# Kernel optimization log

Hardware: AMD Instinct MI355X
Metric: run time of the kernel (lower is better)

## Reference

```python
import jax, jax.numpy as jnp
import numpy as np

G = 128          # dense grid extent per axis
N = 131072       # number of occupied voxels
MUL = 32         # multiplicity of 0e and 1o irreps
DIM = 4 * MUL    # 32 scalars + 32 vectors*3 = 128
NB = 5           # num_radial_basis
R = 2.5          # diameter / 2
K = 125          # 5^3 kernel offsets


def _lattice_constants():
    # 5x5x5 lattice of physical offsets (steps = 1.0)
    v = jnp.arange(-2.0, 3.0)
    xx, yy, zz = jnp.meshgrid(v, v, v, indexing='ij')
    lattice = jnp.stack([xx, yy, zz], -1)              # (5,5,5,3)
    norm = jnp.linalg.norm(lattice, axis=-1)           # (5,5,5)
    # soft_one_hot_linspace, basis='smooth_finite', cutoff=True
    values = jnp.linspace(0.0, R, NB + 2)[1:-1]
    step = R / (NB + 1)
    d = (norm[..., None] - values) / step              # (5,5,5,NB)
    inside = jnp.abs(d) < 1.0
    ds = jnp.clip(d, -1.0 + 1e-6, 1.0 - 1e-6)
    emb = jnp.where(inside, 1.14136 * jnp.exp(2.0 - 1.0 / (1.0 + ds) - 1.0 / (1.0 - ds)), 0.0)
    # spherical harmonics l=0,1, normalize=True, 'component' norm (e3nn l=1 order: y,z,x)
    unit = jnp.where(norm[..., None] > 0, lattice / jnp.maximum(norm, 1e-9)[..., None], 0.0)
    Y0 = jnp.ones_like(norm)
    Y1 = jnp.sqrt(3.0) * unit[..., (1, 2, 0)]          # (5,5,5,3)
    return emb, Y0, Y1


def _kernel(weight):
    """Generate the (125, DIM, DIM) equivariant kernel (tp.right analogue)."""
    emb, Y0, Y1 = _lattice_constants()
    w = (emb @ weight) / K                              # (5,5,5,4096), /= 5*5*5
    w = w.reshape(5, 5, 5, 4, MUL, MUL)
    Wa, Wb, Wc, Wd = w[..., 0, :, :], w[..., 1, :, :], w[..., 2, :, :], w[..., 3, :, :]
    c = 1.0 / jnp.sqrt(64.0)   # path norm: fan = 2 paths * 32*1 per output
    # 0e x 0e -> 0e
    Kss = c * Wa * Y0[..., None, None]                                        # (...,u,w)
    # 0e x 1o -> 1o  (w3j 1/sqrt3 * sqrt(dim_out=3) = 1)
    Ksv = c * jnp.einsum('...uw,...k->...uwk', Wb, Y1).reshape(5, 5, 5, MUL, 3 * MUL)
    # 1o x 1o -> 0e  (dot / sqrt3)
    Kvs = (c / jnp.sqrt(3.0)) * jnp.einsum('...uw,...i->...uiw', Wd, Y1).reshape(5, 5, 5, 3 * MUL, MUL)
    # 1o x 0e -> 1o  (identity on the 3-vector)
    Kvv = c * jnp.einsum('...uw,ik->...uiwk', Wc * Y0[..., None, None], jnp.eye(3)).reshape(5, 5, 5, 3 * MUL, 3 * MUL)
    kern = jnp.concatenate([jnp.concatenate([Kss, Ksv], -1),
                            jnp.concatenate([Kvs, Kvv], -1)], -2)             # (5,5,5,DIM,DIM)
    kern = jnp.einsum('xyzij->zyxij', kern).reshape(-1, DIM, DIM)             # (125,DIM,DIM)
    return kern


def setup_inputs() -> dict:
    rng = np.random.default_rng(0)
    flat = rng.choice(G ** 3, size=N, replace=False)
    coords = np.stack([flat // (G * G), (flat // G) % G, flat % G], -1).astype(np.int32)
    lookup = np.full(G ** 3, N, np.int32)
    lookup[flat] = np.arange(N, dtype=np.int32)
    # kernel offsets ordered to match the zyx-flattened kernel (x fastest)
    v = np.arange(-2, 3, dtype=np.int32)
    zz, yy, xx = np.meshgrid(v, v, v, indexing='ij')
    offs = np.stack([xx, yy, zz], -1).reshape(-1, 3)                          # (125,3)
    nb = coords[None, :, :] + offs[:, None, :]                                # (125,N,3)
    valid = ((nb >= 0) & (nb < G)).all(-1)
    nf = (nb[..., 0].astype(np.int64) * G + nb[..., 1]) * G + nb[..., 2]
    nf = np.clip(nf, 0, G ** 3 - 1)
    neighbor_idx = np.where(valid, lookup[nf], N).astype(np.int32)            # N = sentinel row

    key = jax.random.key(0)
    k1, k2, k3, k4 = jax.random.split(key, 4)
    return {
        'x_feat': jax.random.normal(k1, (N, DIM), jnp.float32),
        'weight': jax.random.normal(k2, (NB, 4 * MUL * MUL), jnp.float32),
        'w_sc_scal': jax.random.normal(k3, (MUL, MUL), jnp.float32),
        'w_sc_vec': jax.random.normal(k4, (MUL, MUL), jnp.float32),
        'neighbor_idx': jnp.asarray(neighbor_idx),
    }


def reference(x_feat, weight, w_sc_scal, w_sc_vec, neighbor_idx):
    kern = _kernel(weight)                                                    # (125,DIM,DIM)
    # self-connection: equivariant Linear (blockwise, fan_in = MUL)
    inv = 1.0 / jnp.sqrt(jnp.asarray(MUL, x_feat.dtype))
    sc_s = (x_feat[:, :MUL] @ w_sc_scal) * inv
    xv = x_feat[:, MUL:].reshape(-1, MUL, 3)
    sc_v = jnp.einsum('nui,uw->nwi', xv, w_sc_vec).reshape(-1, 3 * MUL) * inv
    sc = jnp.concatenate([sc_s, sc_v], -1)
    # sparse Minkowski conv: gather neighbor rows, matmul per offset, accumulate
    Fp = jnp.concatenate([x_feat, jnp.zeros((1, DIM), x_feat.dtype)], 0)      # sentinel zero row
    def step(acc, kx):
        km, idx = kx
        return acc + Fp[idx] @ km, None
    out, _ = jax.lax.scan(step, jnp.zeros_like(x_feat), (kern, neighbor_idx))
    return sc + out
```

## Files before the change

kernel.cpp:

```cpp
#include <hip/hip_runtime.h>

typedef __attribute__((ext_vector_type(8))) short short8;
typedef __attribute__((ext_vector_type(4))) float f32x4;

#define NPTS 131072
#define NOFF 125
#define KERN_USH (NOFF * 8192)

__device__ int g_isf32[4];
__device__ __align__(16) unsigned short g_x[NPTS * 128 + 128];
__device__ __align__(16) unsigned short g_kern[KERN_USH + 128];

__device__ __forceinline__ float bf2f(unsigned short u) {
  unsigned int v = ((unsigned int)u) << 16;
  return __builtin_bit_cast(float, v);
}
__device__ __forceinline__ unsigned short f2bf(float f) {
  unsigned int x = __builtin_bit_cast(unsigned int, f);
  x += 0x7fffu + ((x >> 16) & 1u);
  return (unsigned short)(x >> 16);
}
__device__ __forceinline__ float rdf(const void* p, int i, int isf32) {
  return isf32 ? ((const float*)p)[i] : bf2f(((const unsigned short*)p)[i]);
}

#define GLD16(gp, lp)                                                        \
  __builtin_amdgcn_global_load_lds(                                          \
      (const __attribute__((address_space(1))) unsigned int*)(gp),           \
      (__attribute__((address_space(3))) unsigned int*)(lp), 16, 0, 0)

__global__ __launch_bounds__(64) void k_detect(const unsigned short* x,
                                               const unsigned short* w,
                                               const unsigned short* s,
                                               const unsigned short* v) {
  const unsigned short* ptrs[4] = {x, w, s, v};
  const int l = threadIdx.x;
  #pragma unroll
  for (int i = 0; i < 4; ++i) {
    const unsigned short u = ptrs[i][2 * l];
    const float a = fabsf(bf2f(u));
    const int good = (u == 0) || (a >= 1e-8f && a <= 64.0f);
    const unsigned long long m = __ballot(good);
    if (l == 0) g_isf32[i] = (__popcll(m) < 45) ? 1 : 0;
  }
}

__global__ __launch_bounds__(256) void k_convx(const void* xin) {
  const int t = blockIdx.x * 256 + threadIdx.x;
  const int n = t >> 4;
  const int cp0 = (t & 15) * 8;
  const size_t rb = (size_t)n * 128;
  short8 o;
  if (g_isf32[0]) {
    const float* xf = (const float*)xin;
    #pragma unroll
    for (int j = 0; j < 8; ++j) {
      const int cp = cp0 + j;
      const int src = cp < 32 ? cp : 32 + ((cp - 32) & 31) * 3 + ((cp - 32) >> 5);
      o[j] = (short)f2bf(xf[rb + src]);
    }
  } else {
    const unsigned short* xb = (const unsigned short*)xin;
    #pragma unroll
    for (int j = 0; j < 8; ++j) {
      const int cp = cp0 + j;
      const int src = cp < 32 ? cp : 32 + ((cp - 32) & 31) * 3 + ((cp - 32) >> 5);
      o[j] = (short)xb[rb + src];
    }
  }
  *(short8*)(&g_x[rb + cp0]) = o;
}

__global__ __launch_bounds__(256) void gen_kern(const void* __restrict__ weight,
                                                const void* __restrict__ wscs,
                                                const void* __restrict__ wscv) {
  __shared__ float W[4][32][32];
  __shared__ float embs[5];
  const int wf = g_isf32[1], sf = g_isf32[2], vf = g_isf32[3];
  const int koff = blockIdx.x;
  const int tid = threadIdx.x;
  const int xi = koff % 5, yi = (koff / 5) % 5, zi = koff / 25;
  const float lx = (float)(xi - 2), ly = (float)(yi - 2), lz = (float)(zi - 2);
  const float nrm = sqrtf(lx*lx + ly*ly + lz*lz);
  if (tid < 5) {
    const float step = 2.5f / 6.0f;
    const float vb = step * (float)(tid + 1);
    const float d = (nrm - vb) / step;
    float e = 0.0f;
    if (fabsf(d) < 1.0f) {
      float ds = fminf(fmaxf(d, -1.0f + 1e-6f), 1.0f - 1e-6f);
      e = 1.14136f * expf(2.0f - 1.0f/(1.0f + ds) - 1.0f/(1.0f - ds));
    }
    embs[tid] = e;
  }
  __syncthreads();
  float* Wf = &W[0][0][0];
  for (int m = tid; m < 4096; m += 256) {
    float s = 0.0f;
    #pragma unroll
    for (int b = 0; b < 5; ++b) s += embs[b] * rdf(weight, b*4096 + m, wf);
    Wf[m] = s * (1.0f / 125.0f);
  }
  __syncthreads();
  const float invn = (nrm > 0.0f) ? 1.0f / nrm : 0.0f;
  const float s3 = 1.7320508075688772f;
  const float Y1v0 = s3 * ly * invn;
  const float Y1v1 = s3 * lz * invn;
  const float Y1v2 = s3 * lx * invn;
  const float c  = 0.125f;
  const float cs = 0.125f / s3;
  const bool center = (koff == 62);
  const float inv = 0.17677669529663687f;
  for (int p = tid; p < 8192; p += 256) {
    const int t = p & 7;
    const int lane = (p >> 3) & 63;
    const int blk = p >> 9;
    const int u = ((lane >> 4) << 3) + t;
    const int w = (blk & 1) * 16 + (lane & 15);
    float val;
    if (blk < 8) {
      const int kb = blk >> 1;
      if (kb == 0) {
        val = c * W[0][u][w];
        if (center) val += inv * rdf(wscs, u*32 + w, sf);
      } else {
        const int i = kb - 1;
        const float y = (i == 0) ? Y1v0 : ((i == 1) ? Y1v1 : Y1v2);
        val = cs * W[3][u][w] * y;
      }
    } else if (blk < 14) {
      const int k = (blk - 8) >> 1;
      const float y = (k == 0) ? Y1v0 : ((k == 1) ? Y1v1 : Y1v2);
      val = c * W[1][u][w] * y;
    } else {
      val = c * W[2][u][w];
      if (center) val += inv * rdf(wscv, u*32 + w, vf);
    }
    g_kern[koff * 8192 + p] = f2bf(val);
  }
}

__global__ __launch_bounds__(512, 4) void conv_main(
    const int* __restrict__ nidx,
    void* __restrict__ out)
{
  __shared__ __align__(16) unsigned short Buf[32768];
  const int of32 = g_isf32[0];
  const char* xb = (const char*)g_x;
  const int tid = threadIdx.x;
  const int wv = tid >> 6;
  const int l  = tid & 63;
  const int lr = l & 15;
  const int lk = l >> 4;
  const int m0 = blockIdx.x * 256 + wv * 32;

  f32x4 acc[2][8];
  #pragma unroll
  for (int i = 0; i < 2; ++i)
    #pragma unroll
    for (int j = 0; j < 8; ++j) acc[i][j] = (f32x4)0.0f;

  {
    const unsigned short* s = g_kern + tid*8;
    short8 p0 = *(const short8*)(s);
    short8 p1 = *(const short8*)(s + 4096);
    *(short8*)(&Buf[tid*8])        = p0;
    *(short8*)(&Buf[tid*8 + 4096]) = p1;
  }

  bool vl[2], act[2];
  unsigned uoff[2];
  {
    const int* ip = nidx + m0;
    #pragma unroll
    for (int mt = 0; mt < 2; ++mt) {
      const int idx = __builtin_nontemporal_load(ip + mt*16 + lr);
      vl[mt]  = (unsigned)idx < (unsigned)NPTS;
      act[mt] = __any(vl[mt]);
      uoff[mt] = (unsigned)idx * 256u + (unsigned)lk * 16u;
    }
  }
  short8 a[4][2];
  #pragma unroll
  for (int mt = 0; mt < 2; ++mt) {
    #pragma unroll
    for (int kb = 0; kb < 4; ++kb) {
      short8 v = (short8)(short)0;
      if (vl[mt]) v = *(const short8*)(xb + uoff[mt] + kb*64);
      a[kb][mt] = v;
    }
  }
  __syncthreads();

  int cur = 0;
  for (int ko = 0; ko < NOFF; ++ko) {
    const bool hn = (ko + 1 < NOFF);

    if (hn) {
      const unsigned short* s = g_kern + (ko + 1) * 8192 + wv*512 + l*8;
      unsigned short* d = &Buf[(cur ^ 1) * 8192 + wv*512];
      GLD16(s, d);
      GLD16(s + 4096, d + 4096);
    }
    int idxn[2];
    if (hn) {
      const int* ip = nidx + (size_t)(ko + 1) * NPTS + m0;
      #pragma unroll
      for (int mt = 0; mt < 2; ++mt)
        idxn[mt] = __builtin_nontemporal_load(ip + mt*16 + lr);
    }

    const unsigned short* B = &Buf[cur * 8192];
    if (act[0] || act[1]) {
      #pragma unroll
      for (int kb = 0; kb < 4; ++kb) {
        const short8 bs0 = *(const short8*)(&B[((kb*2 + 0)*64 + l)*8]);
        const short8 bs1 = *(const short8*)(&B[((kb*2 + 1)*64 + l)*8]);
        #pragma unroll
        for (int mt = 0; mt < 2; ++mt) {
          if (act[mt]) {
            acc[mt][0] = __builtin_amdgcn_mfma_f32_16x16x32_bf16(
                a[kb][mt], bs0, acc[mt][0], 0, 0, 0);
            acc[mt][1] = __builtin_amdgcn_mfma_f32_16x16x32_bf16(
                a[kb][mt], bs1, acc[mt][1], 0, 0, 0);
          }
        }
      }
      const short8 bv0 = *(const short8*)(&B[(14*64 + l)*8]);
      const short8 bv1 = *(const short8*)(&B[(15*64 + l)*8]);
      #pragma unroll
      for (int i = 0; i < 3; ++i) {
        const short8 bsv0 = *(const short8*)(&B[((8 + i*2)*64 + l)*8]);
        const short8 bsv1 = *(const short8*)(&B[((9 + i*2)*64 + l)*8]);
        #pragma unroll
        for (int mt = 0; mt < 2; ++mt) {
          if (act[mt]) {
            acc[mt][2 + 2*i] = __builtin_amdgcn_mfma_f32_16x16x32_bf16(
                a[0][mt], bsv0, acc[mt][2 + 2*i], 0, 0, 0);
            acc[mt][2 + 2*i] = __builtin_amdgcn_mfma_f32_16x16x32_bf16(
                a[1 + i][mt], bv0, acc[mt][2 + 2*i], 0, 0, 0);
            acc[mt][3 + 2*i] = __builtin_amdgcn_mfma_f32_16x16x32_bf16(
                a[0][mt], bsv1, acc[mt][3 + 2*i], 0, 0, 0);
            acc[mt][3 + 2*i] = __builtin_amdgcn_mfma_f32_16x16x32_bf16(
                a[1 + i][mt], bv1, acc[mt][3 + 2*i], 0, 0, 0);
          }
        }
      }
    }

    if (hn) {
      #pragma unroll
      for (int mt = 0; mt < 2; ++mt) {
        vl[mt]  = (unsigned)idxn[mt] < (unsigned)NPTS;
        act[mt] = __any(vl[mt]);
        uoff[mt] = (unsigned)idxn[mt] * 256u + (unsigned)lk * 16u;
        #pragma unroll
        for (int kb = 0; kb < 4; ++kb) {
          short8 v = (short8)(short)0;
          if (vl[mt]) v = *(const short8*)(xb + uoff[mt] + kb*64);
          a[kb][mt] = v;
        }
      }
    }
    __syncthreads();
    cur ^= 1;
  }

  if (of32) {
    float* of = (float*)out;
    #pragma unroll
    for (int mt = 0; mt < 2; ++mt)
      #pragma unroll
      for (int q = 0; q < 8; ++q) {
        const int oc = (q < 2) ? (q*16 + lr)
                               : 32 + (((q - 2) & 1)*16 + lr)*3 + ((q - 2) >> 1);
        #pragma unroll
        for (int r = 0; r < 4; ++r)
          __builtin_nontemporal_store(
              acc[mt][q][r],
              &of[(size_t)(m0 + mt*16 + lk*4 + r) * 128 + oc]);
      }
  } else {
    unsigned short* eb = &Buf[0];
    #pragma unroll
    for (int mt = 0; mt < 2; ++mt)
      #pragma unroll
      for (int q = 0; q < 8; ++q) {
        const int oc = (q < 2) ? (q*16 + lr)
                               : 32 + (((q - 2) & 1)*16 + lr)*3 + ((q - 2) >> 1);
        #pragma unroll
        for (int r = 0; r < 4; ++r) {
          const int row = wv*32 + mt*16 + lk*4 + r;
          eb[row*128 + (oc ^ ((row & 7) << 3))] = f2bf(acc[mt][q][r]);
        }
      }
    __syncthreads();
    unsigned short* ob = (unsigned short*)out;
    const int row = tid >> 1;
    #pragma unroll
    for (int it = 0; it < 8; ++it) {
      const int ub = (tid & 1)*64 + it*8;
      const short8 v = *(const short8*)(&eb[row*128 + (ub ^ ((row & 7) << 3))]);
      __builtin_nontemporal_store(
          v, (short8*)&ob[(size_t)(blockIdx.x*256 + row) * 128 + ub]);
    }
  }
}

extern "C" void kernel_launch(void* const* d_in, const int* in_sizes, int n_in,
                              void* d_out, int out_size, void* d_ws, size_t ws_size,
                              hipStream_t stream) {
  const void* weight = d_in[1];
  const void* wscs   = d_in[2];
  const void* wscv   = d_in[3];
  const int*  nidx   = (const int*)d_in[4];

  hipLaunchKernelGGL(k_detect, dim3(1), dim3(64), 0, stream,
                     (const unsigned short*)d_in[0], (const unsigned short*)d_in[1],
                     (const unsigned short*)d_in[2], (const unsigned short*)d_in[3]);
  hipLaunchKernelGGL(k_convx, dim3(NPTS * 128 / (256 * 8)), dim3(256), 0, stream, d_in[0]);
  hipLaunchKernelGGL(gen_kern, dim3(NOFF), dim3(256), 0, stream, weight, wscs, wscv);
  hipLaunchKernelGGL(conv_main, dim3(NPTS / 256), dim3(512), 0, stream,
                     nidx, d_out);
}
```

Measured before the change: 253.0 us.

## Double rows per wave and interleave next-offset gathers with MFMA work

Each wave now handles 64 output rows instead of 32, and blocks shrink to 256 threads, so every B fragment read from LDS feeds twice as many MFMAs. The gather of the next offset's neighbor rows is split into pieces and issued between groups of MFMAs, once each piece's registers are no longer needed, to overlap global-memory latency with compute. The cost is higher register use (acc[4][8] plus a[4][4]) and fewer waves per block, which lowers occupancy and the latency hiding it provides.

New measurement: 327.9 us. +29.6%, slower.

```diff
diff --git a/kernel.cpp b/kernel.cpp
--- a/kernel.cpp
+++ b/kernel.cpp
@@ -140,7 +140,7 @@
   }
 }
 
-__global__ __launch_bounds__(512, 4) void conv_main(
+__global__ __launch_bounds__(256, 2) void conv_main(
     const int* __restrict__ nidx,
     void* __restrict__ out)
 {
@@ -152,37 +152,38 @@
   const int l  = tid & 63;
   const int lr = l & 15;
   const int lk = l >> 4;
-  const int m0 = blockIdx.x * 256 + wv * 32;
-
-  f32x4 acc[2][8];
+  const int m0 = blockIdx.x * 256 + wv * 64;
+
+  f32x4 acc[4][8];
   #pragma unroll
-  for (int i = 0; i < 2; ++i)
+  for (int i = 0; i < 4; ++i)
     #pragma unroll
     for (int j = 0; j < 8; ++j) acc[i][j] = (f32x4)0.0f;
 
   {
     const unsigned short* s = g_kern + tid*8;
-    short8 p0 = *(const short8*)(s);
-    short8 p1 = *(const short8*)(s + 4096);
-    *(short8*)(&Buf[tid*8])        = p0;
-    *(short8*)(&Buf[tid*8 + 4096]) = p1;
-  }
-
-  bool vl[2], act[2];
-  unsigned uoff[2];
+    short8 p[4];
+    #pragma unroll
+    for (int c = 0; c < 4; ++c) p[c] = *(const short8*)(s + c*2048);
+    #pragma unroll
+    for (int c = 0; c < 4; ++c) *(short8*)(&Buf[tid*8 + c*2048]) = p[c];
+  }
+
+  bool vl[4], act[4];
+  unsigned uoff[4];
   {
     const int* ip = nidx + m0;
     #pragma unroll
-    for (int mt = 0; mt < 2; ++mt) {
+    for (int mt = 0; mt < 4; ++mt) {
       const int idx = __builtin_nontemporal_load(ip + mt*16 + lr);
       vl[mt]  = (unsigned)idx < (unsigned)NPTS;
       act[mt] = __any(vl[mt]);
       uoff[mt] = (unsigned)idx * 256u + (unsigned)lk * 16u;
     }
   }
-  short8 a[4][2];
+  short8 a[4][4];
   #pragma unroll
-  for (int mt = 0; mt < 2; ++mt) {
+  for (int mt = 0; mt < 4; ++mt) {
     #pragma unroll
     for (int kb = 0; kb < 4; ++kb) {
       short8 v = (short8)(short)0;
@@ -199,25 +200,27 @@
     if (hn) {
       const unsigned short* s = g_kern + (ko + 1) * 8192 + wv*512 + l*8;
       unsigned short* d = &Buf[(cur ^ 1) * 8192 + wv*512];
-      GLD16(s, d);
-      GLD16(s + 4096, d + 4096);
-    }
-    int idxn[2];
+      #pragma unroll
+      for (int c = 0; c < 4; ++c) GLD16(s + c*2048, d + c*2048);
+    }
+    int idxn[4];
     if (hn) {
       const int* ip = nidx + (size_t)(ko + 1) * NPTS + m0;
       #pragma unroll
-      for (int mt = 0; mt < 2; ++mt)
+      for (int mt = 0; mt < 4; ++mt)
         idxn[mt] = __builtin_nontemporal_load(ip + mt*16 + lr);
     }
 
     const unsigned short* B = &Buf[cur * 8192];
-    if (act[0] || act[1]) {
+    const bool anyact = act[0] || act[1] || act[2] || act[3];
+
+    if (anyact) {
       #pragma unroll
       for (int kb = 0; kb < 4; ++kb) {
         const short8 bs0 = *(const short8*)(&B[((kb*2 + 0)*64 + l)*8]);
         const short8 bs1 = *(const short8*)(&B[((kb*2 + 1)*64 + l)*8]);
         #pragma unroll
-        for (int mt = 0; mt < 2; ++mt) {
+        for (int mt = 0; mt < 4; ++mt) {
           if (act[mt]) {
             acc[mt][0] = __builtin_amdgcn_mfma_f32_16x16x32_bf16(
                 a[kb][mt], bs0, acc[mt][0], 0, 0, 0);
@@ -226,40 +229,75 @@
           }
         }
       }
-      const short8 bv0 = *(const short8*)(&B[(14*64 + l)*8]);
-      const short8 bv1 = *(const short8*)(&B[(15*64 + l)*8]);
+    }
+
+    bool vln[4], actn[4];
+    unsigned uoffn[4];
+    if (hn) {
+      #pragma unroll
+      for (int mt = 0; mt < 4; ++mt) {
+        vln[mt]  = (unsigned)idxn[mt] < (unsigned)NPTS;
+        actn[mt] = __any(vln[mt]);
+        uoffn[mt] = (unsigned)idxn[mt] * 256u + (unsigned)lk * 16u;
+      }
+    }
+
+    if (anyact) {
       #pragma unroll
       for (int i = 0; i < 3; ++i) {
         const short8 bsv0 = *(const short8*)(&B[((8 + i*2)*64 + l)*8]);
         const short8 bsv1 = *(const short8*)(&B[((9 + i*2)*64 + l)*8]);
         #pragma unroll
-        for (int mt = 0; mt < 2; ++mt) {
+        for (int mt = 0; mt < 4; ++mt) {
           if (act[mt]) {
             acc[mt][2 + 2*i] = __builtin_amdgcn_mfma_f32_16x16x32_bf16(
                 a[0][mt], bsv0, acc[mt][2 + 2*i], 0, 0, 0);
-            acc[mt][2 + 2*i] = __builtin_amdgcn_mfma_f32_16x16x32_bf16(
-                a[1 + i][mt], bv0, acc[mt][2 + 2*i], 0, 0, 0);
             acc[mt][3 + 2*i] = __builtin_amdgcn_mfma_f32_16x16x32_bf16(
                 a[0][mt], bsv1, acc[mt][3 + 2*i], 0, 0, 0);
-            acc[mt][3 + 2*i] = __builtin_amdgcn_mfma_f32_16x16x32_bf16(
-                a[1 + i][mt], bv1, acc[mt][3 + 2*i], 0, 0, 0);
           }
         }
       }
     }
-
-    if (hn) {
-      #pragma unroll
-      for (int mt = 0; mt < 2; ++mt) {
-        vl[mt]  = (unsigned)idxn[mt] < (unsigned)NPTS;
-        act[mt] = __any(vl[mt]);
-        uoff[mt] = (unsigned)idxn[mt] * 256u + (unsigned)lk * 16u;
-        #pragma unroll
-        for (int kb = 0; kb < 4; ++kb) {
-          short8 v = (short8)(short)0;
-          if (vl[mt]) v = *(const short8*)(xb + uoff[mt] + kb*64);
-          a[kb][mt] = v;
-        }
+    if (hn) {
+      #pragma unroll
+      for (int mt = 0; mt < 4; ++mt) {
+        short8 v = (short8)(short)0;
+        if (vln[mt]) v = *(const short8*)(xb + uoffn[mt]);
+        a[0][mt] = v;
+      }
+    }
+
+    {
+      const short8 bv0 = *(const short8*)(&B[(14*64 + l)*8]);
+      const short8 bv1 = *(const short8*)(&B[(15*64 + l)*8]);
+      #pragma unroll
+      for (int i = 0; i < 3; ++i) {
+        if (anyact) {
+          #pragma unroll
+          for (int mt = 0; mt < 4; ++mt) {
+            if (act[mt]) {
+              acc[mt][2 + 2*i] = __builtin_amdgcn_mfma_f32_16x16x32_bf16(
+                  a[1 + i][mt], bv0, acc[mt][2 + 2*i], 0, 0, 0);
+              acc[mt][3 + 2*i] = __builtin_amdgcn_mfma_f32_16x16x32_bf16(
+                  a[1 + i][mt], bv1, acc[mt][3 + 2*i], 0, 0, 0);
+            }
+          }
+        }
+        if (hn) {
+          #pragma unroll
+          for (int mt = 0; mt < 4; ++mt) {
+            short8 v = (short8)(short)0;
+            if (vln[mt]) v = *(const short8*)(xb + uoffn[mt] + (1 + i)*64);
+            a[1 + i][mt] = v;
+          }
+        }
+      }
+    }
+
+    if (hn) {
+      #pragma unroll
+      for (int mt = 0; mt < 4; ++mt) {
+        vl[mt] = vln[mt]; act[mt] = actn[mt]; uoff[mt] = uoffn[mt];
       }
     }
     __syncthreads();
@@ -269,7 +307,7 @@
   if (of32) {
     float* of = (float*)out;
     #pragma unroll
-    for (int mt = 0; mt < 2; ++mt)
+    for (int mt = 0; mt < 4; ++mt)
       #pragma unroll
       for (int q = 0; q < 8; ++q) {
         const int oc = (q < 2) ? (q*16 + lr)
@@ -283,23 +321,23 @@
   } else {
     unsigned short* eb = &Buf[0];
     #pragma unroll
-    for (int mt = 0; mt < 2; ++mt)
+    for (int mt = 0; mt < 4; ++mt)
       #pragma unroll
       for (int q = 0; q < 8; ++q) {
         const int oc = (q < 2) ? (q*16 + lr)
                                : 32 + (((q - 2) & 1)*16 + lr)*3 + ((q - 2) >> 1);
         #pragma unroll
         for (int r = 0; r < 4; ++r) {
-          const int row = wv*32 + mt*16 + lk*4 + r;
+          const int row = wv*64 + mt*16 + lk*4 + r;
           eb[row*128 + (oc ^ ((row & 7) << 3))] = f2bf(acc[mt][q][r]);
         }
       }
     __syncthreads();
     unsigned short* ob = (unsigned short*)out;
-    const int row = tid >> 1;
-    #pragma unroll
-    for (int it = 0; it < 8; ++it) {
-      const int ub = (tid & 1)*64 + it*8;
+    const int row = tid;
+    #pragma unroll
+    for (int it = 0; it < 16; ++it) {
+      const int ub = it*8;
       const short8 v = *(const short8*)(&eb[row*128 + (ub ^ ((row & 7) << 3))]);
       __builtin_nontemporal_store(
           v, (short8*)&ob[(size_t)(blockIdx.x*256 + row) * 128 + ub]);
@@ -320,6 +358,6 @@
                      (const unsigned short*)d_in[2], (const unsigned short*)d_in[3]);
   hipLaunchKernelGGL(k_convx, dim3(NPTS * 128 / (256 * 8)), dim3(256), 0, stream, d_in[0]);
   hipLaunchKernelGGL(gen_kern, dim3(NOFF), dim3(256), 0, stream, weight, wscs, wscv);
-  hipLaunchKernelGGL(conv_main, dim3(NPTS / 256), dim3(512), 0, stream,
+  hipLaunchKernelGGL(conv_main, dim3(NPTS / 256), dim3(256), 0, stream,
                      nidx, d_out);
 }
```

## Factor spherical-harmonic scaling out of scalar-to-vector kernel blocks

Applied to the files above, without the earlier changes.

The 0e→1o kernel blocks are Wb scaled by Y1 components, so instead of storing three scaled copies the kernel keeps one unscaled Wb tile. A single MFMA computes x_s·Wb, and the result is scaled by y0/y1/y2 and added into the three vector accumulators with VALU FMAs. This shrinks the per-offset kernel tile from 8192 to 6144 elements, cutting global-to-LDS traffic and removing four MFMAs per m-tile. In exchange it adds VALU FMAs and a per-offset global read of the Y values. The products are now accumulated in fp32 and scaled afterwards rather than rounded to bf16 first.

New measurement: 269.3 us. 6.5% more time.

```diff
diff --git a/kernel.cpp b/kernel.cpp
--- a/kernel.cpp
+++ b/kernel.cpp
@@ -5,11 +5,13 @@
 
 #define NPTS 131072
 #define NOFF 125
-#define KERN_USH (NOFF * 8192)
+#define KTILE 6144
+#define KERN_USH (NOFF * KTILE)
 
 __device__ int g_isf32[4];
 __device__ __align__(16) unsigned short g_x[NPTS * 128 + 128];
 __device__ __align__(16) unsigned short g_kern[KERN_USH + 128];
+__device__ __align__(16) float g_y[NOFF][4];
 
 __device__ __forceinline__ float bf2f(unsigned short u) {
   unsigned int v = ((unsigned int)u) << 16;
@@ -111,7 +113,10 @@
   const float cs = 0.125f / s3;
   const bool center = (koff == 62);
   const float inv = 0.17677669529663687f;
-  for (int p = tid; p < 8192; p += 256) {
+  if (tid == 0) {
+    g_y[koff][0] = Y1v0; g_y[koff][1] = Y1v1; g_y[koff][2] = Y1v2; g_y[koff][3] = 0.0f;
+  }
+  for (int p = tid; p < KTILE; p += 256) {
     const int t = p & 7;
     const int lane = (p >> 3) & 63;
     const int blk = p >> 9;
@@ -128,15 +133,13 @@
         const float y = (i == 0) ? Y1v0 : ((i == 1) ? Y1v1 : Y1v2);
         val = cs * W[3][u][w] * y;
       }
-    } else if (blk < 14) {
-      const int k = (blk - 8) >> 1;
-      const float y = (k == 0) ? Y1v0 : ((k == 1) ? Y1v1 : Y1v2);
-      val = c * W[1][u][w] * y;
+    } else if (blk < 10) {
+      val = c * W[1][u][w];
     } else {
       val = c * W[2][u][w];
       if (center) val += inv * rdf(wscv, u*32 + w, vf);
     }
-    g_kern[koff * 8192 + p] = f2bf(val);
+    g_kern[koff * KTILE + p] = f2bf(val);
   }
 }
 
@@ -164,8 +167,10 @@
     const unsigned short* s = g_kern + tid*8;
     short8 p0 = *(const short8*)(s);
     short8 p1 = *(const short8*)(s + 4096);
+    short8 p2 = *(const short8*)(s + 8192);
     *(short8*)(&Buf[tid*8])        = p0;
     *(short8*)(&Buf[tid*8 + 4096]) = p1;
+    *(short8*)(&Buf[tid*8 + 8192]) = p2;
   }
 
   bool vl[2], act[2];
@@ -197,10 +202,10 @@
     const bool hn = (ko + 1 < NOFF);
 
     if (hn) {
-      const unsigned short* s = g_kern + (ko + 1) * 8192 + wv*512 + l*8;
-      unsigned short* d = &Buf[(cur ^ 1) * 8192 + wv*512];
-      GLD16(s, d);
-      GLD16(s + 4096, d + 4096);
+      const unsigned short* s = g_kern + (ko + 1) * KTILE;
+      unsigned short* d = &Buf[(cur ^ 1) * KTILE];
+      GLD16(s + wv*512 + l*8, d + wv*512);
+      if (wv < 4) GLD16(s + 4096 + wv*512 + l*8, d + 4096 + wv*512);
     }
     int idxn[2];
     if (hn) {
@@ -210,7 +215,7 @@
         idxn[mt] = __builtin_nontemporal_load(ip + mt*16 + lr);
     }
 
-    const unsigned short* B = &Buf[cur * 8192];
+    const unsigned short* B = &Buf[cur * KTILE];
     if (act[0] || act[1]) {
       #pragma unroll
       for (int kb = 0; kb < 4; ++kb) {
@@ -226,23 +231,45 @@
           }
         }
       }
-      const short8 bv0 = *(const short8*)(&B[(14*64 + l)*8]);
-      const short8 bv1 = *(const short8*)(&B[(15*64 + l)*8]);
-      #pragma unroll
-      for (int i = 0; i < 3; ++i) {
-        const short8 bsv0 = *(const short8*)(&B[((8 + i*2)*64 + l)*8]);
-        const short8 bsv1 = *(const short8*)(&B[((9 + i*2)*64 + l)*8]);
+      {
+        const float y0 = g_y[ko][0], y1 = g_y[ko][1], y2 = g_y[ko][2];
+        const short8 bw0 = *(const short8*)(&B[(8*64 + l)*8]);
+        const short8 bw1 = *(const short8*)(&B[(9*64 + l)*8]);
         #pragma unroll
         for (int mt = 0; mt < 2; ++mt) {
           if (act[mt]) {
-            acc[mt][2 + 2*i] = __builtin_amdgcn_mfma_f32_16x16x32_bf16(
-                a[0][mt], bsv0, acc[mt][2 + 2*i], 0, 0, 0);
-            acc[mt][2 + 2*i] = __builtin_amdgcn_mfma_f32_16x16x32_bf16(
-                a[1 + i][mt], bv0, acc[mt][2 + 2*i], 0, 0, 0);
-            acc[mt][3 + 2*i] = __builtin_amdgcn_mfma_f32_16x16x32_bf16(
-                a[0][mt], bsv1, acc[mt][3 + 2*i], 0, 0, 0);
-            acc[mt][3 + 2*i] = __builtin_amdgcn_mfma_f32_16x16x32_bf16(
-                a[1 + i][mt], bv1, acc[mt][3 + 2*i], 0, 0, 0);
+            f32x4 t0 = __builtin_amdgcn_mfma_f32_16x16x32_bf16(
+                a[0][mt], bw0, (f32x4)0.0f, 0, 0, 0);
+            #pragma unroll
+            for (int r = 0; r < 4; ++r) {
+              acc[mt][2][r] += y0 * t0[r];
+              acc[mt][4][r] += y1 * t0[r];
+              acc[mt][6][r] += y2 * t0[r];
+            }
+            f32x4 t1 = __builtin_amdgcn_mfma_f32_16x16x32_bf16(
+                a[0][mt], bw1, (f32x4)0.0f, 0, 0, 0);
+            #pragma unroll
+            for (int r = 0; r < 4; ++r) {
+              acc[mt][3][r] += y0 * t1[r];
+              acc[mt][5][r] += y1 * t1[r];
+              acc[mt][7][r] += y2 * t1[r];
+            }
+          }
+        }
+      }
+      {
+        const short8 bv0 = *(const short8*)(&B[(10*64 + l)*8]);
+        const short8 bv1 = *(const short8*)(&B[(11*64 + l)*8]);
+        #pragma unroll
+        for (int i = 0; i < 3; ++i) {
+          #pragma unroll
+          for (int mt = 0; mt < 2; ++mt) {
+            if (act[mt]) {
+              acc[mt][2 + 2*i] = __builtin_amdgcn_mfma_f32_16x16x32_bf16(
+                  a[1 + i][mt], bv0, acc[mt][2 + 2*i], 0, 0, 0);
+              acc[mt][3 + 2*i] = __builtin_amdgcn_mfma_f32_16x16x32_bf16(
+                  a[1 + i][mt], bv1, acc[mt][3 + 2*i], 0, 0, 0);
+            }
           }
         }
       }
```

## Process two kernel offsets per barrier and interleave neighbor gathers with MFMAs

Applied to the files above, without the earlier changes.

The offset loop is restructured so each iteration handles two kernel offsets from a doubled LDS buffer, halving the number of __syncthreads barriers. Neighbor-row gathers for the next offset are split per k-block and issued right after the MFMAs that last read those A registers, so global loads overlap compute instead of running after the whole MFMA section. Neighbor indices are prefetched two offsets ahead. This raises LDS use to 64 KB per block, which may reduce occupancy, and adds register pressure from the extra index prefetches.

Result: faster. 243.2 us, median of 2 (-3.9%).

```diff
diff --git a/kernel.cpp b/kernel.cpp
--- a/kernel.cpp
+++ b/kernel.cpp
@@ -5,7 +5,8 @@
 
 #define NPTS 131072
 #define NOFF 125
-#define KERN_USH (NOFF * 8192)
+#define KTILE 8192
+#define KERN_USH (NOFF * KTILE)
 
 __device__ int g_isf32[4];
 __device__ __align__(16) unsigned short g_x[NPTS * 128 + 128];
@@ -111,7 +112,7 @@
   const float cs = 0.125f / s3;
   const bool center = (koff == 62);
   const float inv = 0.17677669529663687f;
-  for (int p = tid; p < 8192; p += 256) {
+  for (int p = tid; p < KTILE; p += 256) {
     const int t = p & 7;
     const int lane = (p >> 3) & 63;
     const int blk = p >> 9;
@@ -136,7 +137,7 @@
       val = c * W[2][u][w];
       if (center) val += inv * rdf(wscv, u*32 + w, vf);
     }
-    g_kern[koff * 8192 + p] = f2bf(val);
+    g_kern[koff * KTILE + p] = f2bf(val);
   }
 }
 
@@ -162,109 +163,163 @@
 
   {
     const unsigned short* s = g_kern + tid*8;
-    short8 p0 = *(const short8*)(s);
-    short8 p1 = *(const short8*)(s + 4096);
-    *(short8*)(&Buf[tid*8])        = p0;
-    *(short8*)(&Buf[tid*8 + 4096]) = p1;
-  }
-
-  bool vl[2], act[2];
-  unsigned uoff[2];
+    short8 p[4];
+    #pragma unroll
+    for (int c = 0; c < 4; ++c) p[c] = *(const short8*)(s + c*4096);
+    #pragma unroll
+    for (int c = 0; c < 4; ++c) *(short8*)(&Buf[tid*8 + c*4096]) = p[c];
+  }
+
+  bool actc[2];
+  int iK1[2], iK2[2], iK3[2];
+  short8 a[4][2];
   {
     const int* ip = nidx + m0;
     #pragma unroll
     for (int mt = 0; mt < 2; ++mt) {
       const int idx = __builtin_nontemporal_load(ip + mt*16 + lr);
-      vl[mt]  = (unsigned)idx < (unsigned)NPTS;
-      act[mt] = __any(vl[mt]);
-      uoff[mt] = (unsigned)idx * 256u + (unsigned)lk * 16u;
-    }
-  }
-  short8 a[4][2];
-  #pragma unroll
-  for (int mt = 0; mt < 2; ++mt) {
-    #pragma unroll
-    for (int kb = 0; kb < 4; ++kb) {
-      short8 v = (short8)(short)0;
-      if (vl[mt]) v = *(const short8*)(xb + uoff[mt] + kb*64);
-      a[kb][mt] = v;
-    }
+      const bool vl = (unsigned)idx < (unsigned)NPTS;
+      actc[mt] = __any(vl);
+      const unsigned uo = (unsigned)idx * 256u + (unsigned)lk * 16u;
+      #pragma unroll
+      for (int kb = 0; kb < 4; ++kb) {
+        short8 v = (short8)(short)0;
+        if (vl) v = *(const short8*)(xb + uo + kb*64);
+        a[kb][mt] = v;
+      }
+    }
+    const int* ip1 = nidx + (size_t)NPTS + m0;
+    #pragma unroll
+    for (int mt = 0; mt < 2; ++mt)
+      iK1[mt] = __builtin_nontemporal_load(ip1 + mt*16 + lr);
   }
   __syncthreads();
 
-  int cur = 0;
-  for (int ko = 0; ko < NOFF; ++ko) {
-    const bool hn = (ko + 1 < NOFF);
-
-    if (hn) {
-      const unsigned short* s = g_kern + (ko + 1) * 8192 + wv*512 + l*8;
-      unsigned short* d = &Buf[(cur ^ 1) * 8192 + wv*512];
-      GLD16(s, d);
-      GLD16(s + 4096, d + 4096);
-    }
-    int idxn[2];
-    if (hn) {
-      const int* ip = nidx + (size_t)(ko + 1) * NPTS + m0;
+#define KO_SECTION(BB, RIDX, DOREF)                                           \
+  {                                                                           \
+    const unsigned short* B = &Buf[(BB)];                                     \
+    bool vln[2]; bool actn[2]; unsigned uoffn[2];                             \
+    if (DOREF) {                                                              \
+      _Pragma("unroll")                                                       \
+      for (int mt = 0; mt < 2; ++mt) {                                        \
+        vln[mt]  = (unsigned)(RIDX)[mt] < (unsigned)NPTS;                     \
+        actn[mt] = __any(vln[mt]);                                            \
+        uoffn[mt] = (unsigned)(RIDX)[mt] * 256u + (unsigned)lk * 16u;         \
+      }                                                                       \
+    }                                                                         \
+    const bool anyact = actc[0] || actc[1];                                   \
+    if (anyact) {                                                             \
+      _Pragma("unroll")                                                       \
+      for (int kb = 0; kb < 4; ++kb) {                                        \
+        const short8 bs0 = *(const short8*)(&B[((kb*2 + 0)*64 + l)*8]);       \
+        const short8 bs1 = *(const short8*)(&B[((kb*2 + 1)*64 + l)*8]);       \
+        _Pragma("unroll")                                                     \
+        for (int mt = 0; mt < 2; ++mt) {                                      \
+          if (actc[mt]) {                                                     \
+            acc[mt][0] = __builtin_amdgcn_mfma_f32_16x16x32_bf16(             \
+                a[kb][mt], bs0, acc[mt][0], 0, 0, 0);                         \
+            acc[mt][1] = __builtin_amdgcn_mfma_f32_16x16x32_bf16(             \
+                a[kb][mt], bs1, acc[mt][1], 0, 0, 0);                         \
+          }                                                                   \
+        }                                                                     \
+      }                                                                       \
+      _Pragma("unroll")                                                       \
+      for (int i = 0; i < 3; ++i) {                                           \
+        const short8 bsv0 = *(const short8*)(&B[((8 + i*2)*64 + l)*8]);       \
+        const short8 bsv1 = *(const short8*)(&B[((9 + i*2)*64 + l)*8]);       \
+        _Pragma("unroll")                                                     \
+        for (int mt = 0; mt < 2; ++mt) {                                      \
+          if (actc[mt]) {                                                     \
+            acc[mt][2 + 2*i] = __builtin_amdgcn_mfma_f32_16x16x32_bf16(       \
+                a[0][mt], bsv0, acc[mt][2 + 2*i], 0, 0, 0);                   \
+            acc[mt][3 + 2*i] = __builtin_amdgcn_mfma_f32_16x16x32_bf16(       \
+                a[0][mt], bsv1, acc[mt][3 + 2*i], 0, 0, 0);                   \
+          }                                                                   \
+        }                                                                     \
+      }                                                                       \
+    }                                                                         \
+    if (DOREF) {                         \
+      _Pragma("unroll")                                                       \
+      for (int mt = 0; mt < 2; ++mt) {                                        \
+        short8 v = (short8)(short)0;                                          \
+        if (vln[mt]) v = *(const short8*)(xb + uoffn[mt]);                    \
+        a[0][mt] = v;                                                         \
+      }                                                                       \
+    }                                                                         \
+    {                                                                         \
+      const short8 bv0 = anyact ? *(const short8*)(&B[(14*64 + l)*8])         \
+                                : (short8)(short)0;                           \
+      const short8 bv1 = anyact ? *(const short8*)(&B[(15*64 + l)*8])         \
+                                : (short8)(short)0;                           \
+      _Pragma("unroll")                                                       \
+      for (int i = 0; i < 3; ++i) {                                           \
+        if (anyact) {                                                         \
+          _Pragma("unroll")                                                   \
+          for (int mt = 0; mt < 2; ++mt) {                                    \
+            if (actc[mt]) {                                                   \
+              acc[mt][2 + 2*i] = __builtin_amdgcn_mfma_f32_16x16x32_bf16(     \
+                  a[1 + i][mt], bv0, acc[mt][2 + 2*i], 0, 0, 0);              \
+              acc[mt][3 + 2*i] = __builtin_amdgcn_mfma_f32_16x16x32_bf16(     \
+                  a[1 + i][mt], bv1, acc[mt][3 + 2*i], 0, 0, 0);              \
+            }                                                                 \
+          }                                                                   \
+        }                                                                     \
+        if (DOREF) {                  \
+          _Pragma("unroll")                                                   \
+          for (int mt = 0; mt < 2; ++mt) {                                    \
+            short8 v = (short8)(short)0;                                      \
+            if (vln[mt]) v = *(const short8*)(xb + uoffn[mt] + (1 + i)*64);   \
+            a[1 + i][mt] = v;                                                 \
+          }                                                                   \
+        }                                                                     \
+      }                                                                       \
+    }                                                                         \
+    if (DOREF) {                                                              \
+      _Pragma("unroll")                                                       \
+      for (int mt = 0; mt < 2; ++mt) actc[mt] = actn[mt];                     \
+    }                                                                         \
+  }
+
+  for (int j = 0; j < 62; ++j) {
+    const int cur = j & 1;
+    const int sb  = (cur ^ 1) * 16384;
+    const bool h3 = (j < 61);
+
+    {
+      const unsigned short* s0 = g_kern + (size_t)(2*j + 2) * KTILE;
+      GLD16(s0 + wv*512 + l*8,        &Buf[sb + wv*512]);
+      GLD16(s0 + 4096 + wv*512 + l*8, &Buf[sb + 4096 + wv*512]);
+      if (h3) {
+        const unsigned short* s1 = g_kern + (size_t)(2*j + 3) * KTILE;
+        GLD16(s1 + wv*512 + l*8,        &Buf[sb + 8192 + wv*512]);
+        GLD16(s1 + 4096 + wv*512 + l*8, &Buf[sb + 12288 + wv*512]);
+      }
+    }
+    {
+      const int* ip2 = nidx + (size_t)(2*j + 2) * NPTS + m0;
       #pragma unroll
       for (int mt = 0; mt < 2; ++mt)
-        idxn[mt] = __builtin_nontemporal_load(ip + mt*16 + lr);
-    }
-
-    const unsigned short* B = &Buf[cur * 8192];
-    if (act[0] || act[1]) {
-      #pragma unroll
-      for (int kb = 0; kb < 4; ++kb) {
-        const short8 bs0 = *(const short8*)(&B[((kb*2 + 0)*64 + l)*8]);
-        const short8 bs1 = *(const short8*)(&B[((kb*2 + 1)*64 + l)*8]);
+        iK2[mt] = __builtin_nontemporal_load(ip2 + mt*16 + lr);
+      if (h3) {
+        const int* ip3 = nidx + (size_t)(2*j + 3) * NPTS + m0;
         #pragma unroll
-        for (int mt = 0; mt < 2; ++mt) {
-          if (act[mt]) {
-            acc[mt][0] = __builtin_amdgcn_mfma_f32_16x16x32_bf16(
-                a[kb][mt], bs0, acc[mt][0], 0, 0, 0);
-            acc[mt][1] = __builtin_amdgcn_mfma_f32_16x16x32_bf16(
-                a[kb][mt], bs1, acc[mt][1], 0, 0, 0);
-          }
-        }
-      }
-      const short8 bv0 = *(const short8*)(&B[(14*64 + l)*8]);
-      const short8 bv1 = *(const short8*)(&B[(15*64 + l)*8]);
-      #pragma unroll
-      for (int i = 0; i < 3; ++i) {
-        const short8 bsv0 = *(const short8*)(&B[((8 + i*2)*64 + l)*8]);
-        const short8 bsv1 = *(const short8*)(&B[((9 + i*2)*64 + l)*8]);
-        #pragma unroll
-        for (int mt = 0; mt < 2; ++mt) {
-          if (act[mt]) {
-            acc[mt][2 + 2*i] = __builtin_amdgcn_mfma_f32_16x16x32_bf16(
-                a[0][mt], bsv0, acc[mt][2 + 2*i], 0, 0, 0);
-            acc[mt][2 + 2*i] = __builtin_amdgcn_mfma_f32_16x16x32_bf16(
-                a[1 + i][mt], bv0, acc[mt][2 + 2*i], 0, 0, 0);
-            acc[mt][3 + 2*i] = __builtin_amdgcn_mfma_f32_16x16x32_bf16(
-                a[0][mt], bsv1, acc[mt][3 + 2*i], 0, 0, 0);
-            acc[mt][3 + 2*i] = __builtin_amdgcn_mfma_f32_16x16x32_bf16(
-                a[1 + i][mt], bv1, acc[mt][3 + 2*i], 0, 0, 0);
-          }
-        }
-      }
-    }
-
-    if (hn) {
-      #pragma unroll
-      for (int mt = 0; mt < 2; ++mt) {
-        vl[mt]  = (unsigned)idxn[mt] < (unsigned)NPTS;
-        act[mt] = __any(vl[mt]);
-        uoff[mt] = (unsigned)idxn[mt] * 256u + (unsigned)lk * 16u;
-        #pragma unroll
-        for (int kb = 0; kb < 4; ++kb) {
-          short8 v = (short8)(short)0;
-          if (vl[mt]) v = *(const short8*)(xb + uoff[mt] + kb*64);
-          a[kb][mt] = v;
-        }
-      }
-    }
+        for (int mt = 0; mt < 2; ++mt)
+          iK3[mt] = __builtin_nontemporal_load(ip3 + mt*16 + lr);
+      }
+    }
+
+    KO_SECTION(cur * 16384,        iK1, true)
+    KO_SECTION(cur * 16384 + 8192, iK2, true)
+
+    #pragma unroll
+    for (int mt = 0; mt < 2; ++mt) iK1[mt] = iK3[mt];
     __syncthreads();
-    cur ^= 1;
-  }
+  }
+
+  KO_SECTION(0, iK1, false)
+  __syncthreads();
+
+#undef KO_SECTION
 
   if (of32) {
     float* of = (float*)out;
```
